# Kernel tuning notes

Measured on AMD Instinct MI355X. Metric: run time of the kernel, lower is better.

Reference implementation:

```python
import jax, jax.numpy as jnp
import numpy as np

WIN_SIZE = 11
SIGMA = 1.5
DATA_RANGE = 255.0
C1 = (0.01 * DATA_RANGE) ** 2
C2 = (0.03 * DATA_RANGE) ** 2


def _gauss_1d():
    coords = np.arange(WIN_SIZE, dtype=np.float64) - WIN_SIZE // 2
    g = np.exp(-(coords ** 2) / (2.0 * SIGMA ** 2))
    g = g / g.sum()
    return jnp.asarray(g, dtype=jnp.float32)


def _blur(img, g):
    # Depthwise separable gaussian blur, VALID padding (pytorch_msssim style).
    C = img.shape[1]
    dn = ('NCHW', 'OIHW', 'NCHW')
    kh = jnp.tile(g.reshape(1, 1, WIN_SIZE, 1), (C, 1, 1, 1))  # [C,1,K,1]
    kw = jnp.tile(g.reshape(1, 1, 1, WIN_SIZE), (C, 1, 1, 1))  # [C,1,1,K]
    out = jax.lax.conv_general_dilated(img, kh, (1, 1), 'VALID',
                                       dimension_numbers=dn, feature_group_count=C)
    out = jax.lax.conv_general_dilated(out, kw, (1, 1), 'VALID',
                                       dimension_numbers=dn, feature_group_count=C)
    return out


def _ssim_mean(x, y):
    g = _gauss_1d()
    mu1 = _blur(x, g)
    mu2 = _blur(y, g)
    mu1_sq = mu1 * mu1
    mu2_sq = mu2 * mu2
    mu1_mu2 = mu1 * mu2
    sigma1_sq = _blur(x * x, g) - mu1_sq
    sigma2_sq = _blur(y * y, g) - mu2_sq
    sigma12 = _blur(x * y, g) - mu1_mu2
    cs_map = (2.0 * sigma12 + C2) / (sigma1_sq + sigma2_sq + C2)
    ssim_map = ((2.0 * mu1_mu2 + C1) / (mu1_sq + mu2_sq + C1)) * cs_map
    return jnp.mean(ssim_map)


def setup_inputs() -> dict:
    key = jax.random.key(0)
    kx, ky = jax.random.split(key)
    shape = (16, 3, 512, 512)
    x = jax.random.uniform(kx, shape, dtype=jnp.float32)
    y = jax.random.uniform(ky, shape, dtype=jnp.float32)
    return {"x": x, "y": y, "epoch": 1}


def reference(x, y, epoch):
    # forward computes a Charbonnier L1 too, but it is dead code:
    # loss = ssim_loss = 1 - SSIM(x, y)
    return 1.0 - _ssim_mean(x, y)
```

## Files before the change

### kernel.cpp

```cpp
#include <hip/hip_runtime.h>
#include <math.h>


#define HH 512
#define WW 512
#define NCH 48
#define OUTD 502
#define SEGS 32
#define SEG_ROWS 16
#define ITERS 26
#define NBLK (NCH * SEGS)

#define TWO_C1 13.0050f
#define TWO_C2 117.0450f

struct GW { float g[11]; };

__global__ __launch_bounds__(256, 2)
void ssim_main(const float* __restrict__ x, const float* __restrict__ y,
               float* __restrict__ partial, GW gw) {
    const int tid = threadIdx.x;
    const int bid = blockIdx.x;
    const int ch  = bid >> 5;
    const int seg = bid & (SEGS - 1);
    const int r0  = seg * SEG_ROWS;
    const int nrows = min(SEG_ROWS, OUTD - r0);

    int j = 2 * tid;
    const bool jvalid = (j < OUTD);
    if (!jvalid) j = 500;

    const size_t chbase = (size_t)ch * (HH * WW);
    const float* xb = x + chbase + j;
    const float* yb = y + chbase + j;

    float rP[11][2], rQ[11][2], rS[11][2], rT[11][2];
    float acc = 0.0f;

    #pragma unroll
    for (int it = 0; it < ITERS; ++it) {
        const int s = it % 11;
        const int r = min(r0 + it, HH - 1);
        const float2* xr = (const float2*)(xb + (size_t)r * WW);
        const float2* yr = (const float2*)(yb + (size_t)r * WW);

        float p[12], q[12];
        #pragma unroll
        for (int d = 0; d < 6; ++d) {
            float2 xv = xr[d];
            float2 yv = yr[d];
            p[2*d]   = xv.x + yv.x;  q[2*d]   = xv.x - yv.x;
            p[2*d+1] = xv.y + yv.y;  q[2*d+1] = xv.y - yv.y;
        }

        float hp0=0.f,hq0=0.f,hs0=0.f,ht0=0.f;
        float hp1=0.f,hq1=0.f,hs1=0.f,ht1=0.f;
        #pragma unroll
        for (int k = 0; k < 11; ++k) {
            const float w = gw.g[k];
            const float pk = p[k],   qk = q[k];
            const float pk1 = p[k+1], qk1 = q[k+1];
            hp0 = fmaf(w, pk,      hp0);  hq0 = fmaf(w, qk,      hq0);
            hs0 = fmaf(w, pk*pk,   hs0);  ht0 = fmaf(w, qk*qk,   ht0);
            hp1 = fmaf(w, pk1,     hp1);  hq1 = fmaf(w, qk1,     hq1);
            hs1 = fmaf(w, pk1*pk1, hs1);  ht1 = fmaf(w, qk1*qk1, ht1);
        }
        rP[s][0]=hp0; rP[s][1]=hp1;  rQ[s][0]=hq0; rQ[s][1]=hq1;
        rS[s][0]=hs0; rS[s][1]=hs1;  rT[s][0]=ht0; rT[s][1]=ht1;

        const int il = it - 10;
        if (il >= 0 && il < nrows && jvalid) {
            float P0=0.f,Q0=0.f,S0=0.f,T0=0.f;
            float P1=0.f,Q1=0.f,S1=0.f,T1=0.f;
            #pragma unroll
            for (int k = 0; k < 11; ++k) {
                const int sl = (s + 1 + k) % 11;
                const float w = gw.g[k];
                P0=fmaf(w,rP[sl][0],P0); Q0=fmaf(w,rQ[sl][0],Q0);
                S0=fmaf(w,rS[sl][0],S0); T0=fmaf(w,rT[sl][0],T0);
                P1=fmaf(w,rP[sl][1],P1); Q1=fmaf(w,rQ[sl][1],Q1);
                S1=fmaf(w,rS[sl][1],S1); T1=fmaf(w,rT[sl][1],T1);
            }
            {
                float A = P0*P0, B = Q0*Q0;
                float u1 = A - B, u2 = A + B;
                float ln_ = u1 + TWO_C1;
                float ld_ = u2 + TWO_C1;
                float cn_ = (S0 - T0) - u1 + TWO_C2;
                float cd_ = (S0 + T0) - u2 + TWO_C2;
                acc += __fdividef(ln_ * cn_, ld_ * cd_);
            }
            {
                float A = P1*P1, B = Q1*Q1;
                float u1 = A - B, u2 = A + B;
                float ln_ = u1 + TWO_C1;
                float ld_ = u2 + TWO_C1;
                float cn_ = (S1 - T1) - u1 + TWO_C2;
                float cd_ = (S1 + T1) - u2 + TWO_C2;
                acc += __fdividef(ln_ * cn_, ld_ * cd_);
            }
        }
    }

    #pragma unroll
    for (int off = 32; off > 0; off >>= 1) acc += __shfl_down(acc, off);
    __shared__ float sh[4];
    const int wid  = tid >> 6;
    const int lane = tid & 63;
    if (lane == 0) sh[wid] = acc;
    __syncthreads();
    if (tid == 0) partial[bid] = sh[0] + sh[1] + sh[2] + sh[3];
}

__global__ void ssim_reduce(const float* __restrict__ partial,
                            float* __restrict__ out) {
    double s = 0.0;
    for (int i = threadIdx.x; i < NBLK; i += 256) s += (double)partial[i];
    #pragma unroll
    for (int off = 32; off > 0; off >>= 1) s += __shfl_down(s, off);
    __shared__ double sh[4];
    const int wid  = threadIdx.x >> 6;
    const int lane = threadIdx.x & 63;
    if (lane == 0) sh[wid] = s;
    __syncthreads();
    if (threadIdx.x == 0) {
        double tot = sh[0] + sh[1] + sh[2] + sh[3];
        double cnt = (double)NCH * (double)OUTD * (double)OUTD;
        out[0] = (float)(1.0 - tot / cnt);
    }
}

extern "C" void kernel_launch(void* const* d_in, const int* in_sizes, int n_in,
                              void* d_out, int out_size, void* d_ws, size_t ws_size,
                              hipStream_t stream) {
    const float* x = (const float*)d_in[0];
    const float* y = (const float*)d_in[1];
    float* out = (float*)d_out;
    float* ws  = (float*)d_ws;

    GW gw;
    {
        double v[11], sum = 0.0;
        for (int k = 0; k < 11; ++k) {
            double c = (double)(k - 5);
            v[k] = exp(-(c * c) / 4.5);
            sum += v[k];
        }
        for (int k = 0; k < 11; ++k) gw.g[k] = (float)(v[k] / sum);
    }

    hipLaunchKernelGGL(ssim_main, dim3(NBLK), dim3(256), 0, stream, x, y, ws, gw);
    hipLaunchKernelGGL(ssim_reduce, dim3(1), dim3(256), 0, stream, ws, out);
}
```

Before: 188.4 us.

## Stage input rows in double-buffered LDS with cooperative float4 prefetch

Each block now loads every image row once with coalesced float4 reads, computes the sum and difference planes while writing them to shared memory, and double-buffers them so the next row's global load overlaps the current row's blur. Threads then read their 12-wide horizontal window from LDS instead of doing six overlapping float2 global loads each. This removes redundant global and L1 traffic from the overlapping windows. In exchange it adds a block-wide barrier per row and 8 KB of LDS per block, and it holds the prefetched values in extra registers.

```diff
diff --git a/kernel.cpp b/kernel.cpp
--- a/kernel.cpp
+++ b/kernel.cpp
@@ -19,6 +19,8 @@
 __global__ __launch_bounds__(256, 2)
 void ssim_main(const float* __restrict__ x, const float* __restrict__ y,
                float* __restrict__ partial, GW gw) {
+    __shared__ float lds[2][2][WW];
+
     const int tid = threadIdx.x;
     const int bid = blockIdx.x;
     const int ch  = bid >> 5;
@@ -29,28 +31,51 @@
     int j = 2 * tid;
     const bool jvalid = (j < OUTD);
     if (!jvalid) j = 500;
+    const int tcol = j >> 1;
 
     const size_t chbase = (size_t)ch * (HH * WW);
-    const float* xb = x + chbase + j;
-    const float* yb = y + chbase + j;
+    const float* xc = x + chbase;
+    const float* yc = y + chbase;
+
+    const int isq   = (tid >> 7) & 1;
+    const int chunk = tid & 127;
 
     float rP[11][2], rQ[11][2], rS[11][2], rT[11][2];
     float acc = 0.0f;
 
+    {
+        float4 xv = ((const float4*)(xc + (size_t)r0 * WW))[chunk];
+        float4 yv = ((const float4*)(yc + (size_t)r0 * WW))[chunk];
+        float4 w;
+        if (isq == 0) { w.x=xv.x+yv.x; w.y=xv.y+yv.y; w.z=xv.z+yv.z; w.w=xv.w+yv.w; }
+        else          { w.x=xv.x-yv.x; w.y=xv.y-yv.y; w.z=xv.z-yv.z; w.w=xv.w-yv.w; }
+        ((float4*)&lds[0][isq][0])[chunk] = w;
+    }
+    __syncthreads();
+
     #pragma unroll
     for (int it = 0; it < ITERS; ++it) {
-        const int s = it % 11;
-        const int r = min(r0 + it, HH - 1);
-        const float2* xr = (const float2*)(xb + (size_t)r * WW);
-        const float2* yr = (const float2*)(yb + (size_t)r * WW);
+        const int par = it & 1;
+        const int s   = it % 11;
+
+        float4 xv, yv;
+        if (it < ITERS - 1) {
+            const int rn = min(r0 + it + 1, HH - 1);
+            xv = ((const float4*)(xc + (size_t)rn * WW))[chunk];
+            yv = ((const float4*)(yc + (size_t)rn * WW))[chunk];
+        }
 
         float p[12], q[12];
-        #pragma unroll
-        for (int d = 0; d < 6; ++d) {
-            float2 xv = xr[d];
-            float2 yv = yr[d];
-            p[2*d]   = xv.x + yv.x;  q[2*d]   = xv.x - yv.x;
-            p[2*d+1] = xv.y + yv.y;  q[2*d+1] = xv.y - yv.y;
+        {
+            const float2* pb = (const float2*)&lds[par][0][0];
+            const float2* qb = (const float2*)&lds[par][1][0];
+            #pragma unroll
+            for (int k2 = 0; k2 < 6; ++k2) {
+                float2 pv = pb[tcol + k2];
+                float2 qv = qb[tcol + k2];
+                p[2*k2] = pv.x; p[2*k2+1] = pv.y;
+                q[2*k2] = qv.x; q[2*k2+1] = qv.y;
+            }
         }
 
         float hp0=0.f,hq0=0.f,hs0=0.f,ht0=0.f;
@@ -100,6 +125,14 @@
                 acc += __fdividef(ln_ * cn_, ld_ * cd_);
             }
         }
+
+        if (it < ITERS - 1) {
+            float4 w;
+            if (isq == 0) { w.x=xv.x+yv.x; w.y=xv.y+yv.y; w.z=xv.z+yv.z; w.w=xv.w+yv.w; }
+            else          { w.x=xv.x-yv.x; w.y=xv.y-yv.y; w.z=xv.z-yv.z; w.w=xv.w-yv.w; }
+            ((float4*)&lds[par^1][isq][0])[chunk] = w;
+        }
+        __syncthreads();
     }
 
     #pragma unroll
```

After: 174.5 us. -7.4%, faster.
